# Optimization experiments

Hardware: AMD Instinct MI355X
Metric: run time of the kernel (lower is better)

Reference implementation:

```python
import jax, jax.numpy as jnp
import numpy as np

D = 1024
H = 16
DK = D // H
HID = 4096
EPS = 1e-5


def setup_inputs() -> dict:
    key = jax.random.key(0)
    ks = jax.random.split(key, 16)
    B, S = 2, 2048
    sc = lambda fan_in: 1.0 / np.sqrt(fan_in)
    inp = {
        "x": jax.random.normal(ks[0], (B, S, D), jnp.float32),
        "y": jax.random.normal(ks[1], (B, S, D), jnp.float32),
        "mask": jnp.ones((B, 1, 1, S), jnp.int32),
        # attention projections, stored [in, out]
        "Wq": jax.random.normal(ks[2], (D, D), jnp.float32) * sc(D),
        "bq": jnp.zeros((D,), jnp.float32),
        "Wk": jax.random.normal(ks[3], (D, D), jnp.float32) * sc(D),
        "bk": jnp.zeros((D,), jnp.float32),
        "Wv": jax.random.normal(ks[4], (D, D), jnp.float32) * sc(D),
        "bv": jnp.zeros((D,), jnp.float32),
        "Wo": jax.random.normal(ks[5], (D, D), jnp.float32) * sc(D),
        "bo": jnp.zeros((D,), jnp.float32),
        # FFN
        "W1": jax.random.normal(ks[6], (D, HID), jnp.float32) * sc(D),
        "b1": jnp.zeros((HID,), jnp.float32),
        "W2": jax.random.normal(ks[7], (HID, D), jnp.float32) * sc(HID),
        "b2": jnp.zeros((D,), jnp.float32),
        # LayerNorms
        "g1": jnp.ones((D,), jnp.float32),
        "be1": jnp.zeros((D,), jnp.float32),
        "g2": jnp.ones((D,), jnp.float32),
        "be2": jnp.zeros((D,), jnp.float32),
    }
    return inp


def _layer_norm(x, g, b):
    m = jnp.mean(x, axis=-1, keepdims=True)
    v = jnp.mean(jnp.square(x - m), axis=-1, keepdims=True)
    return (x - m) * jax.lax.rsqrt(v + EPS) * g + b


def _split_heads(t):  # [B,S,D] -> [B,H,S,DK]
    B, S, _ = t.shape
    return t.reshape(B, S, H, DK).transpose(0, 2, 1, 3)


def reference(x, y, mask, Wq, bq, Wk, bk, Wv, bv, Wo, bo,
              W1, b1, W2, b2, g1, be1, g2, be2):
    scale = 1.0 / np.sqrt(DK)
    Q = _split_heads(x @ Wq + bq)
    K = _split_heads(y @ Wk + bk)
    V = _split_heads(y @ Wv + bv)
    scores = jnp.einsum("bhqd,bhkd->bhqk", Q, K) * scale  # [B,H,S,S]
    scores = jnp.where(mask == 0, jnp.float32(-1e9), scores)
    probs = jax.nn.softmax(scores, axis=-1)
    attn = jnp.einsum("bhqk,bhkd->bhqd", probs, V)
    B, _, S, _ = attn.shape
    attn = attn.transpose(0, 2, 1, 3).reshape(B, S, D)
    mha_out = attn @ Wo + bo
    x1 = _layer_norm(x + mha_out, g1, be1)
    ff = jax.nn.relu(x1 @ W1 + b1) @ W2 + b2
    return _layer_norm(x1 + ff, g2, be2)
```

## Files before the change

### kernel.cpp

```cpp
#include <hip/hip_runtime.h>

#define S_ 2048
#define D_ 1024
#define B_ 2
#define H_ 16
#define DK_ 64
#define HID_ 4096

typedef unsigned short u16;
typedef __attribute__((ext_vector_type(8))) short short8;
typedef __attribute__((ext_vector_type(4))) float f32x4;

#define SLOT(q16, r16) (((q16) * 16) + ((r16) ^ (q16)))

__device__ __forceinline__ float bf2f(u16 u) {
  return __uint_as_float(((unsigned int)u) << 16);
}
__device__ __forceinline__ u16 f2bf(float f) {
  unsigned int x = __float_as_uint(f);
  x += 0x7fff + ((x >> 16) & 1);
  return (u16)(x >> 16);
}
__device__ __forceinline__ unsigned int pk2bf(float lo, float hi) {
  return ((__float_as_uint(lo) + 0x8000u) >> 16) | ((__float_as_uint(hi) + 0x8000u) & 0xffff0000u);
}

__global__ void prep_k(
    const float* __restrict__ Wq, const float* __restrict__ Wk,
    const float* __restrict__ Wv, const float* __restrict__ Wo,
    const float* __restrict__ W1, const float* __restrict__ W2,
    u16* __restrict__ WqT, u16* __restrict__ WkT, u16* __restrict__ WvT,
    u16* __restrict__ WoT, u16* __restrict__ W1T, u16* __restrict__ W2T) {
  const int z = blockIdx.z;
  __shared__ u16 tile[32][33];
  const float* in; u16* outp; int R, C;
  switch (z) {
    case 0: in = Wq; outp = WqT; R = 1024; C = 1024; break;
    case 1: in = Wk; outp = WkT; R = 1024; C = 1024; break;
    case 2: in = Wv; outp = WvT; R = 1024; C = 1024; break;
    case 3: in = Wo; outp = WoT; R = 1024; C = 1024; break;
    case 4: in = W1; outp = W1T; R = 1024; C = 4096; break;
    default: in = W2; outp = W2T; R = 4096; C = 1024; break;
  }
  int c0, r0;
  if (z == 5) { c0 = blockIdx.y * 32; r0 = blockIdx.x * 32; }
  else        { c0 = blockIdx.x * 32; r0 = blockIdx.y * 32; }
  if (c0 >= C || r0 >= R) return;
  const int tx = threadIdx.x, ty = threadIdx.y;
  for (int i = ty; i < 32; i += 8)
    tile[i][tx] = f2bf(in[(long)(r0 + i) * C + c0 + tx]);
  __syncthreads();
  for (int i = ty; i < 32; i += 8)
    outp[(long)(c0 + i) * R + r0 + tx] = tile[tx][i];
}

__global__ __launch_bounds__(256) void cvt2_k(const float* __restrict__ x, const float* __restrict__ y,
                                              u16* __restrict__ xb, u16* __restrict__ yb) {
  const int z = blockIdx.y;
  const float* in = z ? y : x;
  u16* outp = z ? yb : xb;
  const int i = blockIdx.x * 256 + threadIdx.x;
  float4 v = ((const float4*)in)[i];
  unsigned int lo = (unsigned int)f2bf(v.x) | ((unsigned int)f2bf(v.y) << 16);
  unsigned int hi = (unsigned int)f2bf(v.z) | ((unsigned int)f2bf(v.w) << 16);
  ((uint2*)outp)[i] = make_uint2(lo, hi);
}

template<int MT, int NT, int OUTF32>
__global__ __launch_bounds__(256) void gemm_bt(
    const u16* __restrict__ A, const u16* __restrict__ Bt,
    const float* __restrict__ bias, void* __restrict__ Cv,
    int K, int lda, int ldb, int ldc,
    long sA, long sB, long sC, int relu) {
  constexpr int BM = MT * 32;
  constexpr int BN = NT * 32;
  __shared__ __align__(16) u16 As[BM * 32];
  __shared__ __align__(16) u16 Bs[BN * 32];
  const int z = blockIdx.z;
  A  += (long)z * sA;
  Bt += (long)z * sB;
  const int tid  = threadIdx.x;
  const int lane = tid & 63, wave = tid >> 6;
  const int quad = lane >> 4, l15 = lane & 15;
  const int wm = wave >> 1, wn = wave & 1;
  const u16* Ab = A  + (long)(blockIdx.y * BM) * lda;
  const u16* Bb = Bt + (long)(blockIdx.x * BN) * ldb;

  f32x4 acc[MT][NT];
#pragma unroll
  for (int i = 0; i < MT; ++i)
#pragma unroll
    for (int j = 0; j < NT; ++j) acc[i][j] = (f32x4){0.f, 0.f, 0.f, 0.f};

  const int r0  = tid >> 2;
  const int kk0 = (tid & 3) * 8;

  for (int kt = 0; kt < K; kt += 32) {
#pragma unroll
    for (int p = 0; p < BM / 64; ++p) {
      __builtin_amdgcn_global_load_lds(
          (const __attribute__((address_space(1))) void*)(Ab + (long)(p * 64 + r0) * lda + kt + kk0),
          (__attribute__((address_space(3))) void*)(&As[p * 2048 + tid * 8]), 16, 0, 0);
    }
#pragma unroll
    for (int p = 0; p < BN / 64; ++p) {
      __builtin_amdgcn_global_load_lds(
          (const __attribute__((address_space(1))) void*)(Bb + (long)(p * 64 + r0) * ldb + kt + kk0),
          (__attribute__((address_space(3))) void*)(&Bs[p * 2048 + tid * 8]), 16, 0, 0);
    }
    __syncthreads();
    short8 af[MT], bfr[NT];
#pragma unroll
    for (int mt = 0; mt < MT; ++mt)
      af[mt] = *(const short8*)&As[(wm * (MT * 16) + mt * 16 + l15) * 32 + quad * 8];
#pragma unroll
    for (int nt = 0; nt < NT; ++nt)
      bfr[nt] = *(const short8*)&Bs[(wn * (NT * 16) + nt * 16 + l15) * 32 + quad * 8];
#pragma unroll
    for (int mt = 0; mt < MT; ++mt)
#pragma unroll
      for (int nt = 0; nt < NT; ++nt)
        acc[mt][nt] = __builtin_amdgcn_mfma_f32_16x16x32_bf16(af[mt], bfr[nt], acc[mt][nt], 0, 0, 0);
    __syncthreads();
  }

#pragma unroll
  for (int nt = 0; nt < NT; ++nt) {
    const int col = blockIdx.x * BN + wn * (NT * 16) + nt * 16 + l15;
    const float bvv = bias ? bias[col] : 0.f;
#pragma unroll
    for (int mt = 0; mt < MT; ++mt) {
#pragma unroll
      for (int r = 0; r < 4; ++r) {
        const int row = blockIdx.y * BM + wm * (MT * 16) + mt * 16 + quad * 4 + r;
        float v = acc[mt][nt][r] + bvv;
        if (relu) v = fmaxf(v, 0.f);
        if (OUTF32) ((float*)Cv)[(long)z * sC + (long)row * ldc + col] = v;
        else        ((u16*)Cv)[(long)z * sC + (long)row * ldc + col] = f2bf(v);
      }
    }
  }
}

__global__ __launch_bounds__(256) void qkv_k(
    const u16* __restrict__ xb, const u16* __restrict__ yb,
    const u16* __restrict__ WqT, const u16* __restrict__ WkT, const u16* __restrict__ WvT,
    const float* __restrict__ bq, const float* __restrict__ bk, const float* __restrict__ bv,
    u16* __restrict__ Q, u16* __restrict__ Kp, u16* __restrict__ Vp) {
  __shared__ __align__(16) u16 As[128 * 32];
  __shared__ __align__(16) u16 Bs[128 * 32];
  const int z = blockIdx.z;
  const u16* A  = (z == 0) ? xb : yb;
  const u16* Bt = (z == 0) ? WqT : (z == 1) ? WkT : WvT;
  const float* bias = (z == 0) ? bq : (z == 1) ? bk : bv;
  u16* C = (z == 0) ? Q : (z == 1) ? Kp : Vp;
  const float sc = (z == 0) ? 0.18033688011112042f : 1.0f;
  const int tid  = threadIdx.x;
  const int lane = tid & 63, wave = tid >> 6;
  const int quad = lane >> 4, l15 = lane & 15;
  const int wm = wave >> 1, wn = wave & 1;
  const u16* Ab = A  + (long)(blockIdx.y * 128) * D_;
  const u16* Bb = Bt + (long)(blockIdx.x * 128) * D_;

  f32x4 acc[4][4];
#pragma unroll
  for (int i = 0; i < 4; ++i)
#pragma unroll
    for (int j = 0; j < 4; ++j) acc[i][j] = (f32x4){0.f, 0.f, 0.f, 0.f};

  const int r0  = tid >> 2;
  const int kk0 = (tid & 3) * 8;

  for (int kt = 0; kt < D_; kt += 32) {
#pragma unroll
    for (int p = 0; p < 2; ++p) {
      __builtin_amdgcn_global_load_lds(
          (const __attribute__((address_space(1))) void*)(Ab + (long)(p * 64 + r0) * D_ + kt + kk0),
          (__attribute__((address_space(3))) void*)(&As[p * 2048 + tid * 8]), 16, 0, 0);
      __builtin_amdgcn_global_load_lds(
          (const __attribute__((address_space(1))) void*)(Bb + (long)(p * 64 + r0) * D_ + kt + kk0),
          (__attribute__((address_space(3))) void*)(&Bs[p * 2048 + tid * 8]), 16, 0, 0);
    }
    __syncthreads();
    short8 af[4], bfr[4];
#pragma unroll
    for (int mt = 0; mt < 4; ++mt)
      af[mt] = *(const short8*)&As[(wm * 64 + mt * 16 + l15) * 32 + quad * 8];
#pragma unroll
    for (int nt = 0; nt < 4; ++nt)
      bfr[nt] = *(const short8*)&Bs[(wn * 64 + nt * 16 + l15) * 32 + quad * 8];
#pragma unroll
    for (int mt = 0; mt < 4; ++mt)
#pragma unroll
      for (int nt = 0; nt < 4; ++nt)
        acc[mt][nt] = __builtin_amdgcn_mfma_f32_16x16x32_bf16(af[mt], bfr[nt], acc[mt][nt], 0, 0, 0);
    __syncthreads();
  }

#pragma unroll
  for (int nt = 0; nt < 4; ++nt) {
    const int col = blockIdx.x * 128 + wn * 64 + nt * 16 + l15;
    const float bvv = bias[col];
#pragma unroll
    for (int mt = 0; mt < 4; ++mt) {
#pragma unroll
      for (int r = 0; r < 4; ++r) {
        const int row = blockIdx.y * 128 + wm * 64 + mt * 16 + quad * 4 + r;
        C[(long)row * D_ + col] = f2bf((acc[mt][nt][r] + bvv) * sc);
      }
    }
  }
}

__global__ void vtrans_k(const u16* __restrict__ V, u16* __restrict__ Vt) {
  __shared__ u16 tile[32][33];
  const int bh = blockIdx.z, b = bh >> 4, h = bh & 15;
  const u16* in = V + (long)b * S_ * D_ + h * DK_;
  u16* outp = Vt + (long)bh * DK_ * S_;
  const int s0 = blockIdx.x * 32, d0 = blockIdx.y * 32;
  const int tx = threadIdx.x, ty = threadIdx.y;
  for (int i = ty; i < 32; i += 8)
    tile[i][tx] = in[(long)(s0 + i) * D_ + d0 + tx];
  __syncthreads();
  for (int i = ty; i < 32; i += 8)
    outp[(long)(d0 + i) * S_ + s0 + tx] = tile[tx][i];
}

__global__ __launch_bounds__(256, 4) void flash_k(
    const u16* __restrict__ Q, const u16* __restrict__ Kp, const u16* __restrict__ Vt,
    const int* __restrict__ mask, u16* __restrict__ ctx) {
  __shared__ __align__(16) u16 sQ[8192];
  __shared__ __align__(16) u16 sK[2][2048];
  __shared__ __align__(16) u16 sV[2][2048];
  __shared__ __align__(16) u16 sP[4][1024];

  const int bh = blockIdx.x, qt = blockIdx.y;
  const int b = bh >> 4, h = bh & 15;
  const int tid = threadIdx.x;
  const int w = tid >> 6, lane = tid & 63;
  const int quad = lane >> 4, l15 = lane & 15;

  const u16* Qg  = Q  + ((long)b * S_ + qt * 128) * D_ + h * DK_;
  const u16* Kg  = Kp + (long)b * S_ * D_ + h * DK_;
  const u16* Vtg = Vt + (long)bh * DK_ * S_;
  const int* maskg = mask + (long)b * S_;
  u16* ctxg = ctx + ((long)b * S_ + qt * 128) * D_ + h * DK_;

  const int krow = tid >> 3, kc = tid & 7;
  const u16* kptr = Kg + (long)krow * D_ + kc * 8;
  const int ksw = (((krow >> 4) * 2 + (kc >> 2)) * 64 + SLOT(kc & 3, krow & 15)) * 8;
  const int vrow = tid >> 2, vc = tid & 3;
  const u16* vptr = Vtg + (long)vrow * S_ + vc * 8;
  const int vsw = ((vrow >> 4) * 64 + SLOT(vc, vrow & 15)) * 8;

  uint4 kreg = *(const uint4*)kptr;
  uint4 vreg = *(const uint4*)vptr;

#pragma unroll
  for (int p = 0; p < 4; ++p) {
    const int idx = p * 256 + tid;
    const int row = idx >> 3, cb = idx & 7;
    uint4 v = *(const uint4*)(Qg + (long)row * D_ + cb * 8);
    *(uint4*)&sQ[(((row >> 4) * 2 + (cb >> 2)) * 64 + SLOT(cb & 3, row & 15)) * 8] = v;
  }
  *(uint4*)&sK[0][ksw] = kreg;
  *(uint4*)&sV[0][vsw] = vreg;
  kreg = *(const uint4*)(kptr + 32 * D_);
  vreg = *(const uint4*)(vptr + 32);
  kptr += 64 * D_;
  vptr += 64;
  __syncthreads();

  const int rslot = SLOT(quad, l15) * 8;

  short8 qf[2][2];
#pragma unroll
  for (int mf = 0; mf < 2; ++mf)
#pragma unroll
    for (int kt = 0; kt < 2; ++kt)
      qf[mf][kt] = *(const short8*)&sQ[(((w * 2 + mf) * 2 + kt) * 64) * 8 + rslot];

  float lsum[2] = {0.f, 0.f};
  f32x4 accO[2][4];
#pragma unroll
  for (int i = 0; i < 2; ++i)
#pragma unroll
    for (int j = 0; j < 4; ++j) accO[i][j] = (f32x4){0.f, 0.f, 0.f, 0.f};

  for (int t = 0; t < 64; ++t) {
    if (t) __syncthreads();
    const int buf = t & 1, nb = buf ^ 1;
    if (t < 63) {
      *(uint4*)&sK[nb][ksw] = kreg;
      *(uint4*)&sV[nb][vsw] = vreg;
      if (t < 62) {
        kreg = *(const uint4*)kptr;
        vreg = *(const uint4*)vptr;
        kptr += 32 * D_;
        vptr += 32;
      }
    }
    f32x4 accS[2][2];
#pragma unroll
    for (int i = 0; i < 2; ++i)
#pragma unroll
      for (int j = 0; j < 2; ++j) accS[i][j] = (f32x4){0.f, 0.f, 0.f, 0.f};
#pragma unroll
    for (int kt = 0; kt < 2; ++kt) {
      short8 kf0 = *(const short8*)&sK[buf][(kt * 64) * 8 + rslot];
      short8 kf1 = *(const short8*)&sK[buf][((2 + kt) * 64) * 8 + rslot];
#pragma unroll
      for (int mf = 0; mf < 2; ++mf) {
        accS[0][mf] = __builtin_amdgcn_mfma_f32_16x16x32_bf16(kf0, qf[mf][kt], accS[0][mf], 0, 0, 0);
        accS[1][mf] = __builtin_amdgcn_mfma_f32_16x16x32_bf16(kf1, qf[mf][kt], accS[1][mf], 0, 0, 0);
      }
    }
    const int4 mv0 = *(const int4*)(maskg + t * 32 + quad * 4);
    const int4 mv1 = *(const int4*)(maskg + t * 32 + 16 + quad * 4);
#pragma unroll
    for (int mk = 0; mk < 2; ++mk) {
      const int4 mv = mk ? mv1 : mv0;
      const int qt2 = mk * 2 + (quad >> 1);
      const int j0 = (quad & 1) * 4;
#pragma unroll
      for (int mf = 0; mf < 2; ++mf) {
        float p0 = mv.x ? __builtin_amdgcn_exp2f(accS[mk][mf][0]) : 0.f;
        float p1 = mv.y ? __builtin_amdgcn_exp2f(accS[mk][mf][1]) : 0.f;
        float p2 = mv.z ? __builtin_amdgcn_exp2f(accS[mk][mf][2]) : 0.f;
        float p3 = mv.w ? __builtin_amdgcn_exp2f(accS[mk][mf][3]) : 0.f;
        lsum[mf] += (p0 + p1) + (p2 + p3);
        *(uint2*)&sP[w][(mf * 64 + SLOT(qt2, l15)) * 8 + j0] =
            make_uint2(pk2bf(p0, p1), pk2bf(p2, p3));
      }
    }
    short8 pf0 = *(const short8*)&sP[w][0 + rslot];
    short8 pf1 = *(const short8*)&sP[w][64 * 8 + rslot];
#pragma unroll
    for (int n = 0; n < 4; ++n) {
      short8 vf = *(const short8*)&sV[buf][(n * 64) * 8 + rslot];
      accO[0][n] = __builtin_amdgcn_mfma_f32_16x16x32_bf16(pf0, vf, accO[0][n], 0, 0, 0);
      accO[1][n] = __builtin_amdgcn_mfma_f32_16x16x32_bf16(pf1, vf, accO[1][n], 0, 0, 0);
    }
  }

#pragma unroll
  for (int mf = 0; mf < 2; ++mf) {
    lsum[mf] += __shfl_xor(lsum[mf], 16, 64);
    lsum[mf] += __shfl_xor(lsum[mf], 32, 64);
  }
#pragma unroll
  for (int mf = 0; mf < 2; ++mf) {
    float inv[4];
#pragma unroll
    for (int r = 0; r < 4; ++r)
      inv[r] = 1.f / __shfl(lsum[mf], quad * 4 + r, 64);
#pragma unroll
    for (int n = 0; n < 4; ++n) {
#pragma unroll
      for (int r = 0; r < 4; ++r)
        ctxg[(long)(w * 32 + mf * 16 + quad * 4 + r) * D_ + n * 16 + l15] =
            f2bf(accO[mf][n][r] * inv[r]);
    }
  }
}

__device__ __forceinline__ float block_reduce_sum(float v, float* red) {
#pragma unroll
  for (int off = 32; off; off >>= 1) v += __shfl_down(v, off, 64);
  __syncthreads();
  if ((threadIdx.x & 63) == 0) red[threadIdx.x >> 6] = v;
  __syncthreads();
  return red[0] + red[1] + red[2] + red[3];
}

__global__ __launch_bounds__(256) void addln_fb(const float* __restrict__ A,
    const u16* __restrict__ M0, const u16* __restrict__ M1, const float* __restrict__ bo,
    const float* __restrict__ g, const float* __restrict__ be, u16* __restrict__ outp) {
  __shared__ float red[4];
  const int row = blockIdx.x, tid = threadIdx.x;
  const float4 av = ((const float4*)(A + (long)row * D_))[tid];
  const uint2 m0 = ((const uint2*)(M0 + (long)row * D_))[tid];
  const uint2 m1 = ((const uint2*)(M1 + (long)row * D_))[tid];
  const int c0 = tid * 4;
  float xv[4];
  xv[0] = av.x + bf2f((u16)(m0.x & 0xffff)) + bf2f((u16)(m1.x & 0xffff)) + bo[c0 + 0];
  xv[1] = av.y + bf2f((u16)(m0.x >> 16))    + bf2f((u16)(m1.x >> 16))    + bo[c0 + 1];
  xv[2] = av.z + bf2f((u16)(m0.y & 0xffff)) + bf2f((u16)(m1.y & 0xffff)) + bo[c0 + 2];
  xv[3] = av.w + bf2f((u16)(m0.y >> 16))    + bf2f((u16)(m1.y >> 16))    + bo[c0 + 3];
  float s  = xv[0] + xv[1] + xv[2] + xv[3];
  float ss = xv[0]*xv[0] + xv[1]*xv[1] + xv[2]*xv[2] + xv[3]*xv[3];
  s  = block_reduce_sum(s, red);
  ss = block_reduce_sum(ss, red);
  const float m   = s * (1.0f / 1024.0f);
  const float var = ss * (1.0f / 1024.0f) - m * m;
  const float rs  = rsqrtf(var + 1e-5f);
  float v0 = (xv[0] - m) * rs * g[c0 + 0] + be[c0 + 0];
  float v1 = (xv[1] - m) * rs * g[c0 + 1] + be[c0 + 1];
  float v2 = (xv[2] - m) * rs * g[c0 + 2] + be[c0 + 2];
  float v3 = (xv[3] - m) * rs * g[c0 + 3] + be[c0 + 3];
  unsigned int o01 = (unsigned int)f2bf(v0) | ((unsigned int)f2bf(v1) << 16);
  unsigned int o23 = (unsigned int)f2bf(v2) | ((unsigned int)f2bf(v3) << 16);
  ((uint2*)(outp + (long)row * D_))[tid] = make_uint2(o01, o23);
}

__global__ __launch_bounds__(256) void addln2_bf(const u16* __restrict__ A,
    const u16* __restrict__ F0, const u16* __restrict__ F1, const float* __restrict__ b2,
    const float* __restrict__ g, const float* __restrict__ be, float* __restrict__ outp) {
  __shared__ float red[4];
  const int row = blockIdx.x, tid = threadIdx.x;
  const uint2 av = ((const uint2*)(A + (long)row * D_))[tid];
  const uint2 f0 = ((const uint2*)(F0 + (long)row * D_))[tid];
  const uint2 f1 = ((const uint2*)(F1 + (long)row * D_))[tid];
  const int c0 = tid * 4;
  float xv[4];
  xv[0] = bf2f((u16)(av.x & 0xffff)) + bf2f((u16)(f0.x & 0xffff)) + bf2f((u16)(f1.x & 0xffff)) + b2[c0 + 0];
  xv[1] = bf2f((u16)(av.x >> 16))    + bf2f((u16)(f0.x >> 16))    + bf2f((u16)(f1.x >> 16))    + b2[c0 + 1];
  xv[2] = bf2f((u16)(av.y & 0xffff)) + bf2f((u16)(f0.y & 0xffff)) + bf2f((u16)(f1.y & 0xffff)) + b2[c0 + 2];
  xv[3] = bf2f((u16)(av.y >> 16))    + bf2f((u16)(f0.y >> 16))    + bf2f((u16)(f1.y >> 16))    + b2[c0 + 3];
  float s  = xv[0] + xv[1] + xv[2] + xv[3];
  float ss = xv[0]*xv[0] + xv[1]*xv[1] + xv[2]*xv[2] + xv[3]*xv[3];
  s  = block_reduce_sum(s, red);
  ss = block_reduce_sum(ss, red);
  const float m   = s * (1.0f / 1024.0f);
  const float var = ss * (1.0f / 1024.0f) - m * m;
  const float rs  = rsqrtf(var + 1e-5f);
  float4 o;
  o.x = (xv[0] - m) * rs * g[c0 + 0] + be[c0 + 0];
  o.y = (xv[1] - m) * rs * g[c0 + 1] + be[c0 + 1];
  o.z = (xv[2] - m) * rs * g[c0 + 2] + be[c0 + 2];
  o.w = (xv[3] - m) * rs * g[c0 + 3] + be[c0 + 3];
  ((float4*)(outp + (long)row * D_))[tid] = o;
}

extern "C" void kernel_launch(void* const* d_in, const int* in_sizes, int n_in,
                              void* d_out, int out_size, void* d_ws, size_t ws_size,
                              hipStream_t stream) {
  const float* x   = (const float*)d_in[0];
  const float* y   = (const float*)d_in[1];
  const int* mask  = (const int*)d_in[2];
  const float* Wq = (const float*)d_in[3];  const float* bq = (const float*)d_in[4];
  const float* Wk = (const float*)d_in[5];  const float* bk = (const float*)d_in[6];
  const float* Wv = (const float*)d_in[7];  const float* bv = (const float*)d_in[8];
  const float* Wo = (const float*)d_in[9];  const float* bo = (const float*)d_in[10];
  const float* W1 = (const float*)d_in[11]; const float* b1 = (const float*)d_in[12];
  const float* W2 = (const float*)d_in[13]; const float* b2 = (const float*)d_in[14];
  const float* g1 = (const float*)d_in[15]; const float* be1 = (const float*)d_in[16];
  const float* g2 = (const float*)d_in[17]; const float* be2 = (const float*)d_in[18];
  float* out = (float*)d_out;

  char* w = (char*)d_ws;
  const size_t MB = 1024 * 1024;
  u16* WqT = (u16*)(w + 0 * MB);
  u16* WkT = (u16*)(w + 2 * MB);
  u16* WvT = (u16*)(w + 4 * MB);
  u16* WoT = (u16*)(w + 6 * MB);
  u16* W1T = (u16*)(w + 8 * MB);
  u16* W2T = (u16*)(w + 16 * MB);
  u16* xb  = (u16*)(w + 24 * MB);
  u16* yb  = (u16*)(w + 32 * MB);
  u16* Q   = (u16*)(w + 40 * MB);
  u16* Kp  = (u16*)(w + 48 * MB);
  u16* Vp  = (u16*)(w + 56 * MB);
  u16* Vt  = (u16*)(w + 64 * MB);
  u16* ctx = (u16*)(w + 72 * MB);
  u16* mha = (u16*)(w + 80 * MB);
  u16* x1  = (u16*)(w + 24 * MB);
  u16* h1  = (u16*)(w + 96 * MB);
  u16* ff  = (u16*)(w + 40 * MB);

  prep_k<<<dim3(128, 32, 6), dim3(32, 8), 0, stream>>>(Wq, Wk, Wv, Wo, W1, W2,
      WqT, WkT, WvT, WoT, W1T, W2T);
  cvt2_k<<<dim3(4096, 2), 256, 0, stream>>>(x, y, xb, yb);

  qkv_k<<<dim3(8, 32, 3), 256, 0, stream>>>(xb, yb, WqT, WkT, WvT, bq, bk, bv, Q, Kp, Vp);

  vtrans_k<<<dim3(64, 2, 32), dim3(32, 8), 0, stream>>>(Vp, Vt);

  flash_k<<<dim3(32, 16), 256, 0, stream>>>(Q, Kp, Vt, mask, ctx);

  gemm_bt<4, 4, 0><<<dim3(8, 32, 2), 256, 0, stream>>>(ctx, WoT, nullptr, mha,
      512, 1024, 1024, 1024, 512, 512, (long)4096 * 1024, 0);
  addln_fb<<<dim3(4096), 256, 0, stream>>>(x, mha, mha + (long)4096 * 1024, bo, g1, be1, x1);

  gemm_bt<4, 4, 0><<<dim3(32, 32, 1), 256, 0, stream>>>(x1, W1T, b1, h1,
      1024, 1024, 1024, 4096, 0, 0, 0, 1);
  gemm_bt<4, 4, 0><<<dim3(8, 32, 2), 256, 0, stream>>>(h1, W2T, nullptr, ff,
      2048, 4096, 4096, 1024, 2048, 2048, (long)4096 * 1024, 0);
  addln2_bf<<<dim3(4096), 256, 0, stream>>>(x1, ff, ff + (long)4096 * 1024, b2, g2, be2, out);
}
```

Measured before the change: 413.6 us.

## Use 256x256 direct-to-LDS pipelined GEMM for FFN with 4-way split-K

Adds a 512-thread GEMM kernel with 256x256 tiles that loads A and B straight into LDS via global_load_lds. It keeps a 4-deep LDS ring buffer, synchronised with vmcnt waits and barriers, and raises wave priority around the MFMA block. Both FFN GEMMs now use it, and W2 changes from a 2-way to a 4-way split-K. The final add+LayerNorm kernel therefore sums four bf16 partials. The goal is more data reuse per tile and better overlap of loads with MFMAs, at the cost of 128KB of LDS per block (one block per CU) and extra partial-sum traffic.

```diff
diff --git a/kernel.cpp b/kernel.cpp
--- a/kernel.cpp
+++ b/kernel.cpp
@@ -137,6 +137,104 @@
         if (relu) v = fmaxf(v, 0.f);
         if (OUTF32) ((float*)Cv)[(long)z * sC + (long)row * ldc + col] = v;
         else        ((u16*)Cv)[(long)z * sC + (long)row * ldc + col] = f2bf(v);
+      }
+    }
+  }
+}
+
+template<int RELU>
+__global__ __launch_bounds__(512, 2) void gemm256_k(
+    const u16* __restrict__ A, const u16* __restrict__ Bt,
+    const float* __restrict__ bias, u16* __restrict__ C,
+    int K, int lda, int ldb, int ldc, int kOff, long sC) {
+  __shared__ __align__(16) u16 lds[65536];
+  const int z = blockIdx.z;
+  A  += (long)z * kOff;
+  Bt += (long)z * kOff;
+  const int tid = threadIdx.x;
+  const int lane = tid & 63, w = tid >> 6;
+  const int quad = lane >> 4, l15 = lane & 15;
+  const int wm = w >> 2, wn = w & 3;
+  const int bx = blockIdx.x, by = blockIdx.y;
+
+  const int srow = w * 16 + l15;
+  const u16* a0p = A + (long)(by * 256 + srow) * lda + quad * 8;
+  const u16* a1p = a0p + (long)128 * lda;
+  const u16* b0p = Bt + (long)(bx * 256 + srow) * ldb + quad * 8;
+  const u16* b1p = b0p + (long)128 * ldb;
+
+  f32x4 acc[8][4];
+#pragma unroll
+  for (int i = 0; i < 8; ++i)
+#pragma unroll
+    for (int j = 0; j < 4; ++j) acc[i][j] = (f32x4){0.f, 0.f, 0.f, 0.f};
+
+  auto STAGE = [&](int c) {
+    const int sl = (c & 3) * 8192;
+    const long ko = (long)c * 32;
+    __builtin_amdgcn_global_load_lds(
+        (const __attribute__((address_space(1))) void*)(a0p + ko),
+        (__attribute__((address_space(3))) void*)(&lds[sl + tid * 8]), 16, 0, 0);
+    __builtin_amdgcn_global_load_lds(
+        (const __attribute__((address_space(1))) void*)(a1p + ko),
+        (__attribute__((address_space(3))) void*)(&lds[sl + 4096 + tid * 8]), 16, 0, 0);
+    __builtin_amdgcn_global_load_lds(
+        (const __attribute__((address_space(1))) void*)(b0p + ko),
+        (__attribute__((address_space(3))) void*)(&lds[32768 + sl + tid * 8]), 16, 0, 0);
+    __builtin_amdgcn_global_load_lds(
+        (const __attribute__((address_space(1))) void*)(b1p + ko),
+        (__attribute__((address_space(3))) void*)(&lds[32768 + sl + 4096 + tid * 8]), 16, 0, 0);
+  };
+
+  auto COMPUTE = [&](int t) {
+    const int sl = (t & 3) * 8192;
+    short8 af[8], bfv[4];
+#pragma unroll
+    for (int fr = 0; fr < 8; ++fr)
+      af[fr] = *(const short8*)&lds[sl + ((wm * 8 + fr) * 64 + lane) * 8];
+#pragma unroll
+    for (int fc = 0; fc < 4; ++fc)
+      bfv[fc] = *(const short8*)&lds[32768 + sl + ((wn * 4 + fc) * 64 + lane) * 8];
+    __builtin_amdgcn_s_setprio(1);
+#pragma unroll
+    for (int fr = 0; fr < 8; ++fr)
+#pragma unroll
+      for (int fc = 0; fc < 4; ++fc)
+        acc[fr][fc] = __builtin_amdgcn_mfma_f32_16x16x32_bf16(af[fr], bfv[fc], acc[fr][fc], 0, 0, 0);
+    __builtin_amdgcn_s_setprio(0);
+  };
+
+  const int NT = K >> 5;
+  STAGE(0); STAGE(1); STAGE(2);
+  for (int t = 0; t < NT - 2; ++t) {
+    asm volatile("s_waitcnt vmcnt(8)" ::: "memory");
+    __builtin_amdgcn_s_barrier();
+    __builtin_amdgcn_sched_barrier(0);
+    if (t + 3 < NT) STAGE(t + 3);
+    COMPUTE(t);
+  }
+  asm volatile("s_waitcnt vmcnt(4)" ::: "memory");
+  __builtin_amdgcn_s_barrier();
+  __builtin_amdgcn_sched_barrier(0);
+  COMPUTE(NT - 2);
+  asm volatile("s_waitcnt vmcnt(0)" ::: "memory");
+  __builtin_amdgcn_s_barrier();
+  __builtin_amdgcn_sched_barrier(0);
+  COMPUTE(NT - 1);
+
+  C += (long)z * sC;
+#pragma unroll
+  for (int fc = 0; fc < 4; ++fc) {
+    const int col = bx * 256 + wn * 64 + fc * 16 + l15;
+    const float bvv = bias ? bias[col] : 0.f;
+#pragma unroll
+    for (int fr = 0; fr < 8; ++fr) {
+      const long row = by * 256 + wm * 128 + fr * 16 + quad * 4;
+#pragma unroll
+      for (int r = 0; r < 4; ++r) {
+        float v = acc[fr][fc][r] + bvv;
+        if (RELU) v = fmaxf(v, 0.f);
+        C[(row + r) * ldc + col] = f2bf(v);
       }
     }
   }
@@ -404,19 +502,27 @@
 }
 
 __global__ __launch_bounds__(256) void addln2_bf(const u16* __restrict__ A,
-    const u16* __restrict__ F0, const u16* __restrict__ F1, const float* __restrict__ b2,
+    const u16* __restrict__ F0, const u16* __restrict__ F1,
+    const u16* __restrict__ F2, const u16* __restrict__ F3,
+    const float* __restrict__ b2,
     const float* __restrict__ g, const float* __restrict__ be, float* __restrict__ outp) {
   __shared__ float red[4];
   const int row = blockIdx.x, tid = threadIdx.x;
   const uint2 av = ((const uint2*)(A + (long)row * D_))[tid];
   const uint2 f0 = ((const uint2*)(F0 + (long)row * D_))[tid];
   const uint2 f1 = ((const uint2*)(F1 + (long)row * D_))[tid];
+  const uint2 f2 = ((const uint2*)(F2 + (long)row * D_))[tid];
+  const uint2 f3 = ((const uint2*)(F3 + (long)row * D_))[tid];
   const int c0 = tid * 4;
   float xv[4];
-  xv[0] = bf2f((u16)(av.x & 0xffff)) + bf2f((u16)(f0.x & 0xffff)) + bf2f((u16)(f1.x & 0xffff)) + b2[c0 + 0];
-  xv[1] = bf2f((u16)(av.x >> 16))    + bf2f((u16)(f0.x >> 16))    + bf2f((u16)(f1.x >> 16))    + b2[c0 + 1];
-  xv[2] = bf2f((u16)(av.y & 0xffff)) + bf2f((u16)(f0.y & 0xffff)) + bf2f((u16)(f1.y & 0xffff)) + b2[c0 + 2];
-  xv[3] = bf2f((u16)(av.y >> 16))    + bf2f((u16)(f0.y >> 16))    + bf2f((u16)(f1.y >> 16))    + b2[c0 + 3];
+  xv[0] = bf2f((u16)(av.x & 0xffff)) + bf2f((u16)(f0.x & 0xffff)) + bf2f((u16)(f1.x & 0xffff))
+        + bf2f((u16)(f2.x & 0xffff)) + bf2f((u16)(f3.x & 0xffff)) + b2[c0 + 0];
+  xv[1] = bf2f((u16)(av.x >> 16))    + bf2f((u16)(f0.x >> 16))    + bf2f((u16)(f1.x >> 16))
+        + bf2f((u16)(f2.x >> 16))    + bf2f((u16)(f3.x >> 16))    + b2[c0 + 1];
+  xv[2] = bf2f((u16)(av.y & 0xffff)) + bf2f((u16)(f0.y & 0xffff)) + bf2f((u16)(f1.y & 0xffff))
+        + bf2f((u16)(f2.y & 0xffff)) + bf2f((u16)(f3.y & 0xffff)) + b2[c0 + 2];
+  xv[3] = bf2f((u16)(av.y >> 16))    + bf2f((u16)(f0.y >> 16))    + bf2f((u16)(f1.y >> 16))
+        + bf2f((u16)(f2.y >> 16))    + bf2f((u16)(f3.y >> 16))    + b2[c0 + 3];
   float s  = xv[0] + xv[1] + xv[2] + xv[3];
   float ss = xv[0]*xv[0] + xv[1]*xv[1] + xv[2]*xv[2] + xv[3]*xv[3];
   s  = block_reduce_sum(s, red);
@@ -482,9 +588,10 @@
       512, 1024, 1024, 1024, 512, 512, (long)4096 * 1024, 0);
   addln_fb<<<dim3(4096), 256, 0, stream>>>(x, mha, mha + (long)4096 * 1024, bo, g1, be1, x1);
 
-  gemm_bt<4, 4, 0><<<dim3(32, 32, 1), 256, 0, stream>>>(x1, W1T, b1, h1,
-      1024, 1024, 1024, 4096, 0, 0, 0, 1);
-  gemm_bt<4, 4, 0><<<dim3(8, 32, 2), 256, 0, stream>>>(h1, W2T, nullptr, ff,
-      2048, 4096, 4096, 1024, 2048, 2048, (long)4096 * 1024, 0);
-  addln2_bf<<<dim3(4096), 256, 0, stream>>>(x1, ff, ff + (long)4096 * 1024, b2, g2, be2, out);
-}
+  gemm256_k<1><<<dim3(16, 16, 1), 512, 0, stream>>>(x1, W1T, b1, h1,
+      1024, 1024, 1024, 4096, 0, 0);
+  gemm256_k<0><<<dim3(4, 16, 4), 512, 0, stream>>>(h1, W2T, nullptr, ff,
+      1024, 4096, 4096, 1024, 1024, (long)4096 * 1024);
+  addln2_bf<<<dim3(4096), 256, 0, stream>>>(x1, ff, ff + (long)4096 * 1024,
+      ff + (long)2 * 4096 * 1024, ff + (long)3 * 4096 * 1024, b2, g2, be2, out);
+}
```

New measurement: 393.3 us. 1.05x faster.
